# Kernel tuning notes

Measured on AMD Instinct MI355X. Metric: run time of the kernel, lower is better.

## Reference

```python
import jax, jax.numpy as jnp
import numpy as np
from math import comb

G, NPG, D = 32, 128, 128   # graphs, nodes-per-graph, hidden dim
N = G * NPG                # 4096 nodes per side
E = 65536                  # edges per side (avg degree 16)
K = 6                      # Bernstein order (bern_k)
S, DCONV, DTR = 16, 4, 8   # mamba d_state, d_conv, dt_rank
HE = 27
SIGMAS = [1.0, 10.0, 100.0, 1000.0, 10000.0]


def _leaky(x, s=0.02):
    return jnp.where(x >= 0, x, s * x)


def _bnorm(x, g, b, eps=1e-5):
    m = jnp.mean(x, axis=0)
    v = jnp.var(x, axis=0)
    return (x - m) * jax.lax.rsqrt(v + eps) * g + b


def _bern_prop(x, src, dst, w, temp):
    # BernNet Bern_prop: Bernstein polynomial of sym-normalized Laplacian with weights relu(temp)
    n = x.shape[0]
    temp = jax.nn.relu(temp)
    deg = jax.ops.segment_sum(w, src, num_segments=n)
    dinv = jnp.where(deg > 0, 1.0 / jnp.sqrt(deg + 1e-12), 0.0)
    nw = (w * dinv[src] * dinv[dst])[:, None]
    adj = lambda v: jax.ops.segment_sum(nw * v[src], dst, num_segments=n)
    tmps = [x]
    xv = x
    for _ in range(K):
        xv = xv + adj(xv)          # (2I - L) v = v + A_norm v
        tmps.append(xv)
    out = (comb(K, 0) / 2 ** K) * temp[0] * tmps[K]
    for i in range(K):
        v = tmps[K - i - 1]
        for _ in range(i + 1):
            v = v - adj(v)         # L v = v - A_norm v
        out = out + (comb(K, i + 1) / 2 ** K) * temp[i + 1] * v
    return out


def _mamba(h, in_w, conv_w, conv_b, xproj_w, dt_w, dt_b, A_log, Dp, out_w):
    # Mamba block, d_model=D, expand=1 (d_inner=D), d_state=S, d_conv=DCONV
    Bb, L, _ = h.shape
    xq, z = jnp.split(h @ in_w, 2, axis=-1)             # [B,L,D] each
    xp = jnp.pad(xq, ((0, 0), (DCONV - 1, 0), (0, 0)))  # causal depthwise conv
    xc = conv_b + sum(xp[:, k:k + L, :] * conv_w[:, k] for k in range(DCONV))
    xc = jax.nn.silu(xc)
    dbl = xc @ xproj_w                                  # [B,L,DTR+2S]
    dt = jax.nn.softplus(dbl[..., :DTR] @ dt_w + dt_b)  # [B,L,D]
    Bm = dbl[..., DTR:DTR + S]
    Cm = dbl[..., DTR + S:]
    A = -jnp.exp(A_log)                                 # [D,S]
    dA = jnp.exp(dt[..., None] * A)                     # [B,L,D,S]
    dBx = dt[..., None] * Bm[:, :, None, :] * xc[..., None]

    def step(hs, ins):
        dA_t, dBx_t, C_t = ins
        hs = dA_t * hs + dBx_t
        return hs, jnp.einsum('bds,bs->bd', hs, C_t)

    h0 = jnp.zeros((Bb, D, S), h.dtype)
    _, ys = jax.lax.scan(step, h0, (jnp.swapaxes(dA, 0, 1),
                                    jnp.swapaxes(dBx, 0, 1),
                                    jnp.swapaxes(Cm, 0, 1)))
    y = jnp.swapaxes(ys, 0, 1) + xc * Dp
    return (y * jax.nn.silu(z)) @ out_w


def _xattn(q, k, v, mask):
    a = mask * (q @ k.T) - 1000.0 * (1.0 - mask)
    return jax.nn.softmax(a, axis=1) @ v


def setup_inputs():
    key = jax.random.key(0)
    ks = jax.random.split(key, 32)
    f = jnp.float32
    nrm = lambda k, shp, sc=1.0: jax.random.normal(k, shp, dtype=f) * sc
    h_lig = nrm(ks[0], (N, D), 0.5)
    h_rec = nrm(ks[1], (N, D), 0.5)
    x_lig = nrm(ks[2], (N, 3))
    x_rec = nrm(ks[3], (N, 3))
    he_1 = jax.random.uniform(ks[4], (E, HE), dtype=f)
    he_2 = jax.random.uniform(ks[5], (E, HE), dtype=f)
    g = (jnp.arange(E) // (E // G)).astype(jnp.int32)
    src1 = g * NPG + jax.random.randint(ks[6], (E,), 0, NPG, dtype=jnp.int32)
    dst1 = g * NPG + jax.random.randint(ks[7], (E,), 0, NPG, dtype=jnp.int32)
    src2 = g * NPG + jax.random.randint(ks[8], (E,), 0, NPG, dtype=jnp.int32)
    dst2 = g * NPG + jax.random.randint(ks[9], (E,), 0, NPG, dtype=jnp.int32)
    edge_index_1 = jnp.stack([src1, dst1])
    edge_index_2 = jnp.stack([src2, dst2])
    batch = (jnp.arange(N) // NPG).astype(jnp.int32)
    rng = np.random.default_rng(0)
    def mkperm(src):
        # lexsort([deg + noise, batch]) with batch as primary key
        deg = np.bincount(np.asarray(src), minlength=N).astype(np.float32)
        return jnp.asarray(np.lexsort((deg + rng.random(N).astype(np.float32),
                                       np.asarray(batch))).astype(np.int32))
    perm_1 = mkperm(src1)
    perm_2 = mkperm(src2)
    p = {}
    p['emlp_w1'] = nrm(ks[10], (32, D), 0.1)
    p['emlp_b1'] = jnp.zeros((D,), f)
    p['emlp_bn_g'] = jnp.ones((D,), f)
    p['emlp_bn_b'] = jnp.zeros((D,), f)
    p['emlp_w2'] = nrm(ks[11], (D, 1), 0.1)
    p['emlp_b2'] = jnp.zeros((1,), f)
    p['bern_temp'] = jnp.ones((K + 1,), f)
    p['m_in_w'] = nrm(ks[12], (D, 2 * D), 0.05)
    p['m_conv_w'] = nrm(ks[13], (D, DCONV), 0.2)
    p['m_conv_b'] = jnp.zeros((D,), f)
    p['m_xproj_w'] = nrm(ks[14], (D, DTR + 2 * S), 0.05)
    p['m_dt_w'] = nrm(ks[15], (DTR, D), 0.2)
    p['m_dt_b'] = jnp.full((D,), -4.0, f)
    p['m_A_log'] = jnp.log(jnp.broadcast_to(jnp.arange(1, S + 1, dtype=f), (D, S)))
    p['m_D'] = jnp.ones((D,), f)
    p['m_out_w'] = nrm(ks[16], (D, D), 0.05)
    p['q_w'] = nrm(ks[17], (D, D), 0.05)
    p['k_w'] = nrm(ks[18], (D, D), 0.05)
    p['v_w'] = nrm(ks[19], (D, D), 0.05)
    p['bn1_g'] = jnp.ones((D,), f)
    p['bn1_b'] = jnp.zeros((D,), f)
    p['bn2_g'] = jnp.ones((D,), f)
    p['bn2_b'] = jnp.zeros((D,), f)
    p['ff_w1'] = nrm(ks[20], (D, 2 * D), 0.05)
    p['ff_b1'] = jnp.zeros((2 * D,), f)
    p['ff_w2'] = nrm(ks[21], (2 * D, D), 0.05)
    p['ff_b2'] = jnp.zeros((D,), f)
    return dict(h_lig=h_lig, h_rec=h_rec, x_lig=x_lig, x_rec=x_rec,
                he_1=he_1, he_2=he_2, **p,
                edge_index_1=edge_index_1, edge_index_2=edge_index_2,
                batch_1=batch, batch_2=batch, perm_1=perm_1, perm_2=perm_2)


def reference(h_lig, h_rec, x_lig, x_rec, he_1, he_2,
              emlp_w1, emlp_b1, emlp_bn_g, emlp_bn_b, emlp_w2, emlp_b2,
              bern_temp, m_in_w, m_conv_w, m_conv_b, m_xproj_w, m_dt_w,
              m_dt_b, m_A_log, m_D, m_out_w, q_w, k_w, v_w,
              bn1_g, bn1_b, bn2_g, bn2_b, ff_w1, ff_b1, ff_w2, ff_b2,
              edge_index_1, edge_index_2, batch_1, batch_2, perm_1, perm_2):

    def side(h, x, he, ei, perm):
        src, dst = ei[0], ei[1]
        d2 = jnp.sum((x[src] - x[dst]) ** 2, axis=1, keepdims=True)
        ew = jnp.concatenate([jnp.exp(-d2 / s) for s in SIGMAS], axis=1)  # [E,5]
        t = _leaky(jnp.concatenate([ew, he], axis=1) @ emlp_w1 + emlp_b1)
        t = _bnorm(t, emlp_bn_g, emlp_bn_b)
        w = jax.nn.relu(t @ emlp_w2 + emlp_b2)[:, 0]                      # [E]
        h_local = _bern_prop(h, src, dst, w, bern_temp)
        inv = jnp.argsort(perm)
        hd = h[perm].reshape(G, NPG, D)   # uniform graph sizes -> exact dense batch
        ha = _mamba(hd, m_in_w, m_conv_w, m_conv_b, m_xproj_w, m_dt_w,
                    m_dt_b, m_A_log, m_D, m_out_w).reshape(N, D)[inv]
        return _bnorm(h + h_local + ha, bn1_g, bn1_b)

    hl = side(h_lig, x_lig, he_1, edge_index_1, perm_1)
    hr = side(h_rec, x_rec, he_2, edge_index_2, perm_2)
    mask = (batch_1[:, None] == batch_2[None, :]).astype(hl.dtype)
    cl = _xattn(_leaky(hl @ q_w), _leaky(hr @ k_w), hr @ v_w, mask)
    cr = _xattn(_leaky(hr @ q_w), _leaky(hl @ k_w), hl @ v_w, mask.T)
    hl = hl + cl
    hr = hr + cr
    ff = lambda h: jax.nn.relu(h @ ff_w1 + ff_b1) @ ff_w2 + ff_b2
    hl = _bnorm(hl + ff(hl), bn2_g, bn2_b)
    hr = _bnorm(hr + ff(hr), bn2_g, bn2_b)
    return hl, hr
```

## Files before the change

kernel.cpp:

```cpp
#include <hip/hip_runtime.h>
#include <math.h>

#define G_    32
#define NPG_  128
#define D_    128
#define N_    4096
#define E_    65536
#define ND_   (N_*D_)

#define W_OFF     0
#define DEG_OFF   65536
#define STATS_OFF 69632
#define BUF0      71680
#define HL_OFF    (BUF0 + 0*ND_)
#define HA_OFF    (BUF0 + 1*ND_)
#define X1_OFF    (BUF0 + 2*ND_)
#define HMID_OFF  (BUF0 + 3*ND_)
#define XC_OFF    (BUF0 + 4*ND_)
#define DTB_OFF   (BUF0 + 5*ND_)
#define YB_OFF    (BUF0 + 6*ND_)
#define XZ_OFF    (BUF0 + 7*ND_)
#define DBL_OFF   (BUF0 + 9*ND_)
#define WT_OFF    (DBL_OFF + N_*40)
#define SS_       ((size_t)(WT_OFF + 4096))

__device__ __forceinline__ float leakyf(float x){ return x >= 0.f ? x : 0.02f*x; }
__device__ __forceinline__ float siluf (float x){ return x / (1.f + expf(-x)); }

__device__ __forceinline__ void edge_feat(const float* __restrict__ x,
                                          const float* __restrict__ he,
                                          const int* __restrict__ ei,
                                          int e, float* feat, int& sN, int& dN)
{
  sN = ei[e]; dN = ei[E_ + e];
  float dx = x[sN*3+0]-x[dN*3+0];
  float dy = x[sN*3+1]-x[dN*3+1];
  float dz = x[sN*3+2]-x[dN*3+2];
  float d2 = dx*dx + dy*dy + dz*dz;
  feat[0] = expf(-d2);
  feat[1] = expf(d2 * -0.1f);
  feat[2] = expf(d2 * -0.01f);
  feat[3] = expf(d2 * -0.001f);
  feat[4] = expf(d2 * -0.0001f);
#pragma unroll
  for (int j = 0; j < 27; ++j) feat[5+j] = he[(size_t)e*27 + j];
}

__global__ void wt_kernel(const float* __restrict__ w1, float* __restrict__ wt)
{
  for (int k = threadIdx.x; k < 4096; k += 256) {
    int c = k >> 5, j = k & 31;
    wt[k] = w1[j*128 + c];
  }
}

__global__ __launch_bounds__(256, 2)
void edge_stats_kernel(const float* __restrict__ xl, const float* __restrict__ xr,
                       const float* __restrict__ hel, const float* __restrict__ her,
                       const int* __restrict__ ei1, const int* __restrict__ ei2,
                       const float* __restrict__ wt, const float* __restrict__ b1,
                       float* __restrict__ ws)
{
  int side = blockIdx.y;
  const float* x  = side ? xr  : xl;
  const float* he = side ? her : hel;
  const int*   ei = side ? ei2 : ei1;
  float* stats = ws + (size_t)side*SS_ + STATS_OFF;
  __shared__ float featL[256][36];
  __shared__ float lstat[256];
  int tid = threadIdx.x;

  {
    int sN, dN; float feat[32];
    edge_feat(x, he, ei, blockIdx.x*256 + tid, feat, sN, dN);
#pragma unroll
    for (int j4 = 0; j4 < 8; ++j4)
      *(float4*)&featL[tid][j4*4] = *(float4*)&feat[j4*4];
  }
  lstat[tid] = 0.f;
  __syncthreads();

  int w    = tid >> 6;
  int lane = tid & 63;
  int es   = lane >> 5;
  int cg   = lane & 31;
  float4 wr[4][8];
  float  b1r[4];
#pragma unroll
  for (int c = 0; c < 4; ++c) {
    b1r[c] = b1[4*cg + c];
#pragma unroll
    for (int j4 = 0; j4 < 8; ++j4)
      wr[c][j4] = *(const float4*)&wt[(4*cg + c)*32 + j4*4];
  }
  float s1[4] = {0.f,0.f,0.f,0.f}, s2[4] = {0.f,0.f,0.f,0.f};
  int ebase = w*64 + es*32;
  for (int i = 0; i < 32; ++i) {
    const float* fr = featL[ebase + i];
    float4 f[8];
#pragma unroll
    for (int j4 = 0; j4 < 8; ++j4) f[j4] = *(const float4*)&fr[j4*4];
#pragma unroll
    for (int c = 0; c < 4; ++c) {
      float acc = b1r[c];
#pragma unroll
      for (int j4 = 0; j4 < 8; ++j4) {
        float4 w4 = wr[c][j4];
        acc += f[j4].x*w4.x + f[j4].y*w4.y + f[j4].z*w4.z + f[j4].w*w4.w;
      }
      float t = leakyf(acc);
      s1[c] += t; s2[c] += t*t;
    }
  }
#pragma unroll
  for (int c = 0; c < 4; ++c) {
    s1[c] += __shfl_xor(s1[c], 32, 64);
    s2[c] += __shfl_xor(s2[c], 32, 64);
  }
  if (es == 0) {
#pragma unroll
    for (int c = 0; c < 4; ++c) {
      atomicAdd(&lstat[4*cg + c],       s1[c]);
      atomicAdd(&lstat[128 + 4*cg + c], s2[c]);
    }
  }
  __syncthreads();
  atomicAdd(&stats[tid], lstat[tid]);
}

__global__ void edge_finalize_kernel(const float* __restrict__ g_, const float* __restrict__ b_,
                                     const float* __restrict__ w2, const float* __restrict__ b2,
                                     float* __restrict__ ws)
{
  int side = blockIdx.y;
  float* stats = ws + (size_t)side*SS_ + STATS_OFF;
  __shared__ float red[128];
  int c = threadIdx.x;
  const float invE = 1.f/(float)E_;
  float mean = stats[c]*invE;
  float var  = fmaxf(stats[128+c]*invE - mean*mean, 0.f);
  float scale = rsqrtf(var + 1e-5f) * g_[c];
  stats[256+c] = scale * w2[c];
  red[c] = (b_[c] - mean*scale) * w2[c];
  __syncthreads();
  for (int off = 64; off; off >>= 1) { if (c < off) red[c] += red[c+off]; __syncthreads(); }
  if (c == 0) stats[384] = red[0] + b2[0];
}

__global__ __launch_bounds__(256, 2)
void edge_w_kernel(const float* __restrict__ xl, const float* __restrict__ xr,
                   const float* __restrict__ hel, const float* __restrict__ her,
                   const int* __restrict__ ei1, const int* __restrict__ ei2,
                   const float* __restrict__ wt, const float* __restrict__ b1,
                   float* __restrict__ ws)
{
  int side = blockIdx.y;
  const float* x  = side ? xr  : xl;
  const float* he = side ? her : hel;
  const int*   ei = side ? ei2 : ei1;
  float* base = ws + (size_t)side*SS_;
  const float* stats = base + STATS_OFF;
  float* wbuf = base + W_OFF;
  float* deg  = base + DEG_OFF;
  __shared__ float featL[256][36];
  int tid = threadIdx.x;

  {
    int sN, dN; float feat[32];
    edge_feat(x, he, ei, blockIdx.x*256 + tid, feat, sN, dN);
#pragma unroll
    for (int j4 = 0; j4 < 8; ++j4)
      *(float4*)&featL[tid][j4*4] = *(float4*)&feat[j4*4];
    *(int*)&featL[tid][32] = sN;
  }
  __syncthreads();

  int w    = tid >> 6;
  int lane = tid & 63;
  int es   = lane >> 5;
  int cg   = lane & 31;
  float4 wr[4][8];
  float  b1r[4], al[4];
#pragma unroll
  for (int c = 0; c < 4; ++c) {
    b1r[c] = b1[4*cg + c];
    al[c]  = stats[256 + 4*cg + c];
#pragma unroll
    for (int j4 = 0; j4 < 8; ++j4)
      wr[c][j4] = *(const float4*)&wt[(4*cg + c)*32 + j4*4];
  }
  float beta = stats[384];
  int ebase = w*64 + es*32;
  for (int i = 0; i < 32; ++i) {
    const float* fr = featL[ebase + i];
    float4 f[8];
#pragma unroll
    for (int j4 = 0; j4 < 8; ++j4) f[j4] = *(const float4*)&fr[j4*4];
    float p = 0.f;
#pragma unroll
    for (int c = 0; c < 4; ++c) {
      float acc = b1r[c];
#pragma unroll
      for (int j4 = 0; j4 < 8; ++j4) {
        float4 w4 = wr[c][j4];
        acc += f[j4].x*w4.x + f[j4].y*w4.y + f[j4].z*w4.z + f[j4].w*w4.w;
      }
      p += leakyf(acc) * al[c];
    }
    p += __shfl_xor(p, 1, 32);
    p += __shfl_xor(p, 2, 32);
    p += __shfl_xor(p, 4, 32);
    p += __shfl_xor(p, 8, 32);
    p += __shfl_xor(p, 16, 32);
    if (cg == 0) {
      int e = blockIdx.x*256 + ebase + i;
      float wv = fmaxf(beta + p, 0.f);
      wbuf[e] = wv;
      int sN = *(const int*)&featL[ebase + i][32];
      atomicAdd(&deg[sN], wv);
    }
  }
}

__global__ __launch_bounds__(256)
void bern_horner_kernel(const float* __restrict__ hl_in, const float* __restrict__ hr_in,
                        const int* __restrict__ ei1, const int* __restrict__ ei2,
                        const float* __restrict__ bern_temp, float* __restrict__ ws)
{
  int side = blockIdx.y;
  int g  = blockIdx.x >> 2;
  int d0 = (blockIdx.x & 3) * 32;
  const float* h  = side ? hr_in : hl_in;
  const int*   ei = side ? ei2 : ei1;
  float* base = ws + (size_t)side*SS_;
  const float* wbuf = base + W_OFF;
  const float* deg  = base + DEG_OFF;
  float* hloc = base + HL_OFF;

  __shared__ float A[128*132];
  __shared__ float v[128*32];
  int tid = threadIdx.x;
  for (int i = tid; i < 128*132; i += 256) A[i] = 0.f;

  const float btab[7][7] = {
    { 1,  6, 15,  20, 15,  6,  1},
    { 1,  4,  5,   0, -5, -4, -1},
    { 1,  2, -1,  -4, -1,  2,  1},
    { 1,  0, -3,   0,  3,  0, -1},
    { 1, -2, -1,   4, -1, -2,  1},
    { 1, -4,  5,   0, -5,  4, -1},
    { 1, -6, 15, -20, 15, -6,  1}};
  const float comb6[7] = {1,6,15,20,15,6,1};
  float a[7];
#pragma unroll
  for (int m = 0; m < 7; ++m) a[m] = 0.f;
#pragma unroll
  for (int j = 0; j < 7; ++j) {
    float tj = fmaxf(bern_temp[j], 0.f) * comb6[j] * (1.f/64.f);
#pragma unroll
    for (int m = 0; m < 7; ++m) a[m] += tj * btab[j][m];
  }
  __syncthreads();

  int ebase = g*2048, nbase = g*128;
  for (int i = tid; i < 2048; i += 256) {
    int e = ebase + i;
    int sN = ei[e], dN = ei[E_ + e];
    float ds_ = deg[sN], dd_ = deg[dN];
    float aa = ds_ > 0.f ? rsqrtf(ds_ + 1e-12f) : 0.f;
    float bb = dd_ > 0.f ? rsqrtf(dd_ + 1e-12f) : 0.f;
    atomicAdd(&A[(dN - nbase)*132 + (sN - nbase)], wbuf[e]*aa*bb);
  }

  const int db = (tid & 7)*4;
  const int rb = (tid >> 3)*4;
  float hreg[4][4], r[4][4], t[4][4];
#pragma unroll
  for (int i = 0; i < 4; ++i) {
    float4 h4 = *(const float4*)&h[(size_t)(nbase + rb + i)*128 + d0 + db];
    hreg[i][0]=h4.x; hreg[i][1]=h4.y; hreg[i][2]=h4.z; hreg[i][3]=h4.w;
#pragma unroll
    for (int jj = 0; jj < 4; ++jj) r[i][jj] = a[6]*hreg[i][jj];
  }

  for (int step = 5; step >= 0; --step) {
    __syncthreads();
#pragma unroll
    for (int i = 0; i < 4; ++i)
      *(float4*)&v[(rb+i)*32 + db] = make_float4(r[i][0], r[i][1], r[i][2], r[i][3]);
    __syncthreads();
#pragma unroll
    for (int i = 0; i < 4; ++i)
#pragma unroll
      for (int jj = 0; jj < 4; ++jj) t[i][jj] = 0.f;
    for (int k = 0; k < 128; k += 4) {
      float4 V0 = *(const float4*)&v[(k+0)*32 + db];
      float4 V1 = *(const float4*)&v[(k+1)*32 + db];
      float4 V2 = *(const float4*)&v[(k+2)*32 + db];
      float4 V3 = *(const float4*)&v[(k+3)*32 + db];
#pragma unroll
      for (int i = 0; i < 4; ++i) {
        float4 A4 = *(const float4*)&A[(rb+i)*132 + k];
        t[i][0] += A4.x*V0.x + A4.y*V1.x + A4.z*V2.x + A4.w*V3.x;
        t[i][1] += A4.x*V0.y + A4.y*V1.y + A4.z*V2.y + A4.w*V3.y;
        t[i][2] += A4.x*V0.z + A4.y*V1.z + A4.z*V2.z + A4.w*V3.z;
        t[i][3] += A4.x*V0.w + A4.y*V1.w + A4.z*V2.w + A4.w*V3.w;
      }
    }
    float ak = a[step];
#pragma unroll
    for (int i = 0; i < 4; ++i)
#pragma unroll
      for (int jj = 0; jj < 4; ++jj) r[i][jj] = t[i][jj] + ak*hreg[i][jj];
  }

#pragma unroll
  for (int i = 0; i < 4; ++i)
    *(float4*)&hloc[(size_t)(nbase + rb + i)*128 + d0 + db] =
        make_float4(r[i][0], r[i][1], r[i][2], r[i][3]);
}

template<int K, int NC, int TC, int CSPLIT, int ACT, int GATHER, int SCATTER, int ADDC, int BIAS>
__global__ __launch_bounds__(256)
void gemm_kernel(const float* __restrict__ A0, const float* __restrict__ A1, int lda,
                 const float* __restrict__ W, const float* __restrict__ bias,
                 float* __restrict__ C0, float* __restrict__ C1, int ldc,
                 const int* __restrict__ idx0, const int* __restrict__ idx1,
                 const float* __restrict__ add0, const float* __restrict__ add1)
{
  int side = blockIdx.y;
  const float* A = side ? A1 : A0;
  float* C = side ? C1 : C0;
  const int* idx = side ? idx1 : idx0;
  const float* addsrc = side ? add1 : add0;
  constexpr int RPT = TC/8;
  constexpr int CLEN = NC/CSPLIT;
  __shared__ float Alds[32][K];
  __shared__ float Wlds[K][TC];
  const int tid = threadIdx.x;
  const int r0 = (blockIdx.x / CSPLIT) * 32;
  const int cbase = (blockIdx.x % CSPLIT) * CLEN;
  for (int i = tid*4; i < 32*K; i += 1024) {
    int r = i / K, k = i % K;
    int row = GATHER ? idx[r0 + r] : (r0 + r);
    *(float4*)&Alds[r][k] = *(const float4*)&A[(size_t)row*lda + k];
  }
  for (int c0 = cbase; c0 < cbase + CLEN; c0 += TC) {
    __syncthreads();
    for (int i = tid*4; i < K*TC; i += 1024) {
      int k = i / TC, c = i % TC;
      if (c0 + c < NC) *(float4*)&Wlds[k][c] = *(const float4*)&W[k*NC + c0 + c];
      else             *(float4*)&Wlds[k][c] = make_float4(0.f,0.f,0.f,0.f);
    }
    __syncthreads();
    const int cl = tid % TC;
    const int rsub = (tid / TC) * RPT;
    float accv[RPT];
#pragma unroll
    for (int j = 0; j < RPT; ++j) accv[j] = 0.f;
    for (int k = 0; k < K; k += 4) {
      float w0 = Wlds[k][cl], w1v = Wlds[k+1][cl], w2v = Wlds[k+2][cl], w3v = Wlds[k+3][cl];
#pragma unroll
      for (int j = 0; j < RPT; ++j) {
        float4 a4 = *(const float4*)&Alds[rsub+j][k];
        accv[j] += a4.x*w0 + a4.y*w1v + a4.z*w2v + a4.w*w3v;
      }
    }
    int c = c0 + cl;
    if (c < NC) {
#pragma unroll
      for (int j = 0; j < RPT; ++j) {
        int row  = r0 + rsub + j;
        int orow = SCATTER ? idx[row] : row;
        float vv = accv[j];
        if (BIAS)     vv += bias[c];
        if (ACT == 1) vv = leakyf(vv);
        if (ACT == 2) vv = fmaxf(vv, 0.f);
        if (ADDC)     vv += addsrc[(size_t)orow*ldc + c];
        C[(size_t)orow*ldc + c] = vv;
      }
    }
  }
}

__global__ __launch_bounds__(256)
void qkv_kernel(const float* __restrict__ qw, const float* __restrict__ kw,
                const float* __restrict__ vw, float* __restrict__ ws)
{
  int side = blockIdx.y;
  int mat  = blockIdx.z;
  float* base = ws + (size_t)side*SS_;
  const float* A = base + HMID_OFF;
  const float* W = mat == 0 ? qw : (mat == 1 ? kw : vw);
  float* C = base + (mat == 0 ? XC_OFF : (mat == 1 ? DTB_OFF : YB_OFF));
  __shared__ float Alds[32][128];
  __shared__ float Wlds[128][64];
  const int tid = threadIdx.x;
  const int r0 = (blockIdx.x >> 1) * 32;
  const int c0 = (blockIdx.x & 1) * 64;
  for (int i = tid*4; i < 32*128; i += 1024)
    *(float4*)&Alds[i>>7][i&127] = *(const float4*)&A[(size_t)(r0 + (i>>7))*128 + (i&127)];
  for (int i = tid*4; i < 128*64; i += 1024)
    *(float4*)&Wlds[i>>6][i&63] = *(const float4*)&W[(i>>6)*128 + c0 + (i&63)];
  __syncthreads();
  const int cl = tid & 63;
  const int rsub = (tid >> 6) * 8;
  float accv[8];
#pragma unroll
  for (int j = 0; j < 8; ++j) accv[j] = 0.f;
  for (int k = 0; k < 128; k += 4) {
    float w0 = Wlds[k][cl], w1v = Wlds[k+1][cl], w2v = Wlds[k+2][cl], w3v = Wlds[k+3][cl];
#pragma unroll
    for (int j = 0; j < 8; ++j) {
      float4 a4 = *(const float4*)&Alds[rsub+j][k];
      accv[j] += a4.x*w0 + a4.y*w1v + a4.z*w2v + a4.w*w3v;
    }
  }
#pragma unroll
  for (int j = 0; j < 8; ++j) {
    float vv = accv[j];
    if (mat < 2) vv = leakyf(vv);
    C[(size_t)(r0 + rsub + j)*128 + c0 + cl] = vv;
  }
}

__global__ __launch_bounds__(256)
void conv_kernel(const float* __restrict__ cw, const float* __restrict__ cb, float* __restrict__ ws)
{
  int side = blockIdx.y;
  float* base = ws + (size_t)side*SS_;
  const float* xz = base + XZ_OFF;
  float* xc = base + XC_OFF;
  int i = blockIdx.x*256 + threadIdx.x;
  int j = i >> 7, d = i & 127;
  int l = j & 127;
  float a = cb[d];
#pragma unroll
  for (int k = 0; k < 4; ++k) {
    int ll = l - 3 + k;
    if (ll >= 0) a += xz[(size_t)(j-3+k)*256 + d] * cw[d*4 + k];
  }
  xc[i] = siluf(a);
}

__global__ __launch_bounds__(256)
void scan_kernel(const float* __restrict__ A_log, const float* __restrict__ Dp,
                 const float* __restrict__ dtw, const float* __restrict__ dtbias,
                 float* __restrict__ ws)
{
  int side = blockIdx.z;
  int g  = blockIdx.x;
  int d0 = blockIdx.y * 16;
  float* base = ws + (size_t)side*SS_;
  const float* dbl = base + DBL_OFF;
  const float* xcb = base + XC_OFF;
  float* xz = base + XZ_OFF;

  __shared__ float ldbl[128][40];
  __shared__ float lxc[128][16];
  __shared__ float ldt[128][16];
  __shared__ float lz[128][16];
  __shared__ float ly[128][16];
  __shared__ float ltw[8][16];
  __shared__ float ltb[16];

  int tid = threadIdx.x;
  int rowbase = g*128;
  if (tid < 128)      ltw[tid>>4][tid&15] = dtw[(tid>>4)*128 + d0 + (tid&15)];
  else if (tid < 144) ltb[tid-128] = dtbias[d0 + (tid-128)];
  for (int i = tid; i < 128*40; i += 256)
    ((float*)ldbl)[i] = dbl[(size_t)rowbase*40 + i];
  for (int i = tid; i < 2048; i += 256) {
    int l = i >> 4, dd = i & 15;
    lxc[l][dd] = xcb[(size_t)(rowbase+l)*128 + d0 + dd];
    lz[l][dd]  = xz[(size_t)(rowbase+l)*256 + 128 + d0 + dd];
  }
  __syncthreads();
  for (int i = tid; i < 2048; i += 256) {
    int l = i >> 4, dd = i & 15;
    float a = ltb[dd];
#pragma unroll
    for (int k = 0; k < 8; ++k) a += ldbl[l][k]*ltw[k][dd];
    ldt[l][dd] = a > 20.f ? a : log1pf(expf(a));
  }
  __syncthreads();

  int s = tid & 15, dl = (tid >> 4) & 15;
  float Ac  = -expf(A_log[(d0+dl)*16 + s]);
  float dpv = Dp[d0+dl];
  float hsv = 0.f;
  for (int l = 0; l < 128; ++l) {
    float dtv = ldt[l][dl];
    float xcv = lxc[l][dl];
    float Bv  = ldbl[l][8+s];
    float Cv  = ldbl[l][24+s];
    hsv = expf(dtv*Ac)*hsv + (dtv*xcv)*Bv;
    float val = hsv*Cv;
    val += __shfl_xor(val, 1, 16);
    val += __shfl_xor(val, 2, 16);
    val += __shfl_xor(val, 4, 16);
    val += __shfl_xor(val, 8, 16);
    if (s == 0) ly[l][dl] = val + xcv*dpv;
  }
  __syncthreads();
  for (int i = tid; i < 2048; i += 256) {
    int l = i >> 4, dd = i & 15;
    float y = ly[l][dd];
    float z = lz[l][dd];
    xz[(size_t)(rowbase+l)*256 + d0 + dd] = y * siluf(z);
  }
}

__global__ __launch_bounds__(256)
void stats_kernel(const float* __restrict__ hl_in, const float* __restrict__ hr_in,
                  float* __restrict__ ws, int mode, int statsoff)
{
  int side = blockIdx.y;
  float* base = ws + (size_t)side*SS_;
  const float* h    = side ? hr_in : hl_in;
  const float* hloc = base + HL_OFF;
  const float* ha   = base + HA_OFF;
  float* x1 = base + X1_OFF;
  float* stats = base + STATS_OFF + statsoff;
  int tid = threadIdx.x;
  int c = tid & 127;
  float s1 = 0.f, s2 = 0.f;
  for (int it = 0; it < 16; ++it) {
    int r = blockIdx.x*32 + (tid >> 7) + it*2;
    size_t i = (size_t)r*128 + c;
    float v;
    if (mode == 0) { v = h[i] + hloc[i] + ha[i]; x1[i] = v; }
    else           { v = ha[i]; }
    s1 += v; s2 += v*v;
  }
  __shared__ float red[256];
  red[tid] = s1; __syncthreads();
  if (tid < 128) atomicAdd(&stats[tid], red[tid] + red[tid+128]);
  __syncthreads();
  red[tid] = s2; __syncthreads();
  if (tid < 128) atomicAdd(&stats[128+tid], red[tid] + red[tid+128]);
}

__global__ void bn_finalize_kernel(const float* __restrict__ g_, const float* __restrict__ b_,
                                   float* __restrict__ ws, int statsoff, float invM)
{
  int side = blockIdx.y;
  float* stats = ws + (size_t)side*SS_ + STATS_OFF + statsoff;
  int c = threadIdx.x;
  float mean = stats[c]*invM;
  float var  = fmaxf(stats[128+c]*invM - mean*mean, 0.f);
  float scale = rsqrtf(var + 1e-5f) * g_[c];
  stats[256+c] = scale;
  stats[384+c] = b_[c] - mean*scale;
}

__global__ __launch_bounds__(256)
void bn_apply_kernel(float* __restrict__ ws, float* __restrict__ dout,
                     int srcoff, int dstoff, int statsoff, int to_dout)
{
  int side = blockIdx.y;
  float* base = ws + (size_t)side*SS_;
  const float* src = base + srcoff;
  const float* stats = base + STATS_OFF + statsoff;
  float* dst = to_dout ? (dout + (size_t)side*ND_) : (base + dstoff);
  size_t i = (size_t)blockIdx.x*256 + threadIdx.x;
  int c = (int)(i & 127);
  dst[i] = src[i]*stats[256+c] + stats[384+c];
}

__global__ __launch_bounds__(256)
void attn_kernel(float* __restrict__ ws)
{
  int dir = blockIdx.z;
  int g   = blockIdx.x;
  int rt  = blockIdx.y;
  float* baseq = ws + (size_t)dir*SS_;
  float* basek = ws + (size_t)(1-dir)*SS_;
  const float* qb = baseq + XC_OFF;
  const float* kb = basek + DTB_OFF;
  const float* vb = basek + YB_OFF;
  const float* hm = baseq + HMID_OFF;
  float* h2 = baseq + X1_OFF;

  __shared__ float KT[128][132];
  __shared__ float Qs[32][132];
  __shared__ float sp[32][132];

  const int tid = threadIdx.x;
  const int cl  = tid & 31;
  const int r0  = (tid >> 5) * 4;
  const int c0  = cl * 4;
  const int rowg = g*128 + rt*32;

  {
    const float* qsrc = qb + (size_t)rowg*128;
    for (int i = tid; i < 32*32; i += 256) {
      int r = i >> 5, d4 = i & 31;
      *(float4*)&Qs[r][d4*4] = *(const float4*)&qsrc[(size_t)r*128 + d4*4];
    }
  }
  {
    const float* ksrc = kb + (size_t)(g*128)*128;
    for (int i = tid; i < 128*32; i += 256) {
      int d4 = i >> 7, n = i & 127;
      float4 k4 = *(const float4*)&ksrc[(size_t)n*128 + d4*4];
      KT[d4*4+0][n] = k4.x;
      KT[d4*4+1][n] = k4.y;
      KT[d4*4+2][n] = k4.z;
      KT[d4*4+3][n] = k4.w;
    }
  }
  __syncthreads();

  float acc[4][4];
#pragma unroll
  for (int i = 0; i < 4; ++i)
#pragma unroll
    for (int j = 0; j < 4; ++j) acc[i][j] = 0.f;

  for (int d = 0; d < 128; d += 4) {
    float4 k0 = *(const float4*)&KT[d+0][c0];
    float4 k1 = *(const float4*)&KT[d+1][c0];
    float4 k2 = *(const float4*)&KT[d+2][c0];
    float4 k3 = *(const float4*)&KT[d+3][c0];
#pragma unroll
    for (int i = 0; i < 4; ++i) {
      float4 q4 = *(const float4*)&Qs[r0+i][d];
      acc[i][0] += q4.x*k0.x + q4.y*k1.x + q4.z*k2.x + q4.w*k3.x;
      acc[i][1] += q4.x*k0.y + q4.y*k1.y + q4.z*k2.y + q4.w*k3.y;
      acc[i][2] += q4.x*k0.z + q4.y*k1.z + q4.z*k2.z + q4.w*k3.z;
      acc[i][3] += q4.x*k0.w + q4.y*k1.w + q4.z*k2.w + q4.w*k3.w;
    }
  }

  float inv[4];
#pragma unroll
  for (int i = 0; i < 4; ++i) {
    float m = fmaxf(fmaxf(acc[i][0], acc[i][1]), fmaxf(acc[i][2], acc[i][3]));
#pragma unroll
    for (int off = 1; off < 32; off <<= 1) m = fmaxf(m, __shfl_xor(m, off, 32));
    float p0 = expf(acc[i][0]-m), p1 = expf(acc[i][1]-m);
    float p2 = expf(acc[i][2]-m), p3 = expf(acc[i][3]-m);
    float s = p0 + p1 + p2 + p3;
#pragma unroll
    for (int off = 1; off < 32; off <<= 1) s += __shfl_xor(s, off, 32);
    inv[i] = 1.f/s;
    *(float4*)&sp[r0+i][c0] = make_float4(p0, p1, p2, p3);
  }
  __syncthreads();

  {
    const float* vsrc = vb + (size_t)(g*128)*128;
    for (int i = tid; i < 128*32; i += 256) {
      int n = i >> 5, d4 = i & 31;
      *(float4*)&KT[n][d4*4] = *(const float4*)&vsrc[(size_t)n*128 + d4*4];
    }
  }
  __syncthreads();

  float o[4][4];
#pragma unroll
  for (int i = 0; i < 4; ++i)
#pragma unroll
    for (int j = 0; j < 4; ++j) o[i][j] = 0.f;

  for (int n = 0; n < 128; n += 4) {
    float4 v0 = *(const float4*)&KT[n+0][c0];
    float4 v1 = *(const float4*)&KT[n+1][c0];
    float4 v2 = *(const float4*)&KT[n+2][c0];
    float4 v3 = *(const float4*)&KT[n+3][c0];
#pragma unroll
    for (int i = 0; i < 4; ++i) {
      float4 p4 = *(const float4*)&sp[r0+i][n];
      o[i][0] += p4.x*v0.x + p4.y*v1.x + p4.z*v2.x + p4.w*v3.x;
      o[i][1] += p4.x*v0.y + p4.y*v1.y + p4.z*v2.y + p4.w*v3.y;
      o[i][2] += p4.x*v0.z + p4.y*v1.z + p4.z*v2.z + p4.w*v3.z;
      o[i][3] += p4.x*v0.w + p4.y*v1.w + p4.z*v2.w + p4.w*v3.w;
    }
  }

#pragma unroll
  for (int i = 0; i < 4; ++i) {
    size_t off = (size_t)(rowg + r0 + i)*128 + c0;
    float4 hm4 = *(const float4*)&hm[off];
    float4 r4;
    r4.x = hm4.x + o[i][0]*inv[i];
    r4.y = hm4.y + o[i][1]*inv[i];
    r4.z = hm4.z + o[i][2]*inv[i];
    r4.w = hm4.w + o[i][3]*inv[i];
    *(float4*)&h2[off] = r4;
  }
}

extern "C" void kernel_launch(void* const* d_in, const int* in_sizes, int n_in,
                              void* d_out, int out_size, void* d_ws, size_t ws_size,
                              hipStream_t stream)
{
  const float* h_lig     = (const float*)d_in[0];
  const float* h_rec     = (const float*)d_in[1];
  const float* x_lig     = (const float*)d_in[2];
  const float* x_rec     = (const float*)d_in[3];
  const float* he_1      = (const float*)d_in[4];
  const float* he_2      = (const float*)d_in[5];
  const float* emlp_w1   = (const float*)d_in[6];
  const float* emlp_b1   = (const float*)d_in[7];
  const float* emlp_bn_g = (const float*)d_in[8];
  const float* emlp_bn_b = (const float*)d_in[9];
  const float* emlp_w2   = (const float*)d_in[10];
  const float* emlp_b2   = (const float*)d_in[11];
  const float* bern_temp = (const float*)d_in[12];
  const float* m_in_w    = (const float*)d_in[13];
  const float* m_conv_w  = (const float*)d_in[14];
  const float* m_conv_b  = (const float*)d_in[15];
  const float* m_xproj_w = (const float*)d_in[16];
  const float* m_dt_w    = (const float*)d_in[17];
  const float* m_dt_b    = (const float*)d_in[18];
  const float* m_A_log   = (const float*)d_in[19];
  const float* m_D       = (const float*)d_in[20];
  const float* m_out_w   = (const float*)d_in[21];
  const float* q_w       = (const float*)d_in[22];
  const float* k_w       = (const float*)d_in[23];
  const float* v_w       = (const float*)d_in[24];
  const float* bn1_g     = (const float*)d_in[25];
  const float* bn1_b     = (const float*)d_in[26];
  const float* bn2_g     = (const float*)d_in[27];
  const float* bn2_b     = (const float*)d_in[28];
  const float* ff_w1     = (const float*)d_in[29];
  const float* ff_b1     = (const float*)d_in[30];
  const float* ff_w2     = (const float*)d_in[31];
  const float* ff_b2     = (const float*)d_in[32];
  const int*   ei1       = (const int*)d_in[33];
  const int*   ei2       = (const int*)d_in[34];
  const int*   perm1     = (const int*)d_in[37];
  const int*   perm2     = (const int*)d_in[38];

  float* ws   = (float*)d_ws;
  float* dout = (float*)d_out;

#define B0(off) (ws + (size_t)(off))
#define B1(off) (ws + SS_ + (size_t)(off))

  for (int s = 0; s < 2; ++s)
    hipMemsetAsync((char*)d_ws + ((size_t)s*SS_ + DEG_OFF)*sizeof(float), 0,
                   (N_ + 2048)*sizeof(float), stream);

  wt_kernel<<<1, 256, 0, stream>>>(emlp_w1, B0(WT_OFF));
  edge_stats_kernel<<<dim3(256,2), 256, 0, stream>>>(x_lig,x_rec,he_1,he_2,ei1,ei2,B0(WT_OFF),emlp_b1,ws);
  edge_finalize_kernel<<<dim3(1,2), 128, 0, stream>>>(emlp_bn_g,emlp_bn_b,emlp_w2,emlp_b2,ws);
  edge_w_kernel<<<dim3(256,2), 256, 0, stream>>>(x_lig,x_rec,he_1,he_2,ei1,ei2,B0(WT_OFF),emlp_b1,ws);

  bern_horner_kernel<<<dim3(G_*4,2), 256, 0, stream>>>(h_lig,h_rec,ei1,ei2,bern_temp,ws);

  gemm_kernel<128,256,64,4,0,1,0,0,0><<<dim3(512,2),256,0,stream>>>(
      h_lig,h_rec,128, m_in_w,nullptr, B0(XZ_OFF),B1(XZ_OFF),256, perm1,perm2, nullptr,nullptr);
  conv_kernel<<<dim3(2048,2), 256, 0, stream>>>(m_conv_w,m_conv_b,ws);
  gemm_kernel<128,40,64,1,0,0,0,0,0><<<dim3(128,2),256,0,stream>>>(
      B0(XC_OFF),B1(XC_OFF),128, m_xproj_w,nullptr, B0(DBL_OFF),B1(DBL_OFF),40, nullptr,nullptr, nullptr,nullptr);
  scan_kernel<<<dim3(32,8,2), 256, 0, stream>>>(m_A_log,m_D,m_dt_w,m_dt_b,ws);
  gemm_kernel<128,128,64,2,0,0,1,0,0><<<dim3(256,2),256,0,stream>>>(
      B0(XZ_OFF),B1(XZ_OFF),256, m_out_w,nullptr, B0(HA_OFF),B1(HA_OFF),128, perm1,perm2, nullptr,nullptr);

  stats_kernel<<<dim3(128,2), 256, 0, stream>>>(h_lig,h_rec,ws,0,512);
  bn_finalize_kernel<<<dim3(1,2), 128, 0, stream>>>(bn1_g,bn1_b,ws,512,1.f/(float)N_);
  bn_apply_kernel<<<dim3(2048,2), 256, 0, stream>>>(ws,dout,X1_OFF,HMID_OFF,512,0);

  qkv_kernel<<<dim3(256,2,3), 256, 0, stream>>>(q_w,k_w,v_w,ws);
  attn_kernel<<<dim3(32,4,2), 256, 0, stream>>>(ws);

  gemm_kernel<128,256,64,4,2,0,0,0,1><<<dim3(512,2),256,0,stream>>>(
      B0(X1_OFF),B1(X1_OFF),128, ff_w1,ff_b1, B0(XZ_OFF),B1(XZ_OFF),256, nullptr,nullptr, nullptr,nullptr);
  gemm_kernel<256,128,32,4,0,0,0,1,1><<<dim3(512,2),256,0,stream>>>(
      B0(XZ_OFF),B1(XZ_OFF),256, ff_w2,ff_b2, B0(HA_OFF),B1(HA_OFF),128, nullptr,nullptr, B0(X1_OFF),B1(X1_OFF));
  stats_kernel<<<dim3(128,2), 256, 0, stream>>>(h_lig,h_rec,ws,1,1024);
  bn_finalize_kernel<<<dim3(1,2), 128, 0, stream>>>(bn2_g,bn2_b,ws,1024,1.f/(float)N_);
  bn_apply_kernel<<<dim3(2048,2), 256, 0, stream>>>(ws,dout,HA_OFF,0,1024,1);
}
```

Baseline: 457.7 us.

## Register-tile edge MLP over 4x4 blocks and cache edge features between passes

The edge MLP first layer in both edge kernels is restructured so that each thread computes a 4-edge by 4-channel tile, with the weight matrix staged in shared memory instead of per-thread registers. The transpose kernel goes away. The stats pass now writes the 32-float edge features to a workspace buffer (aliased onto the h_local region), and the weight pass reloads them instead of recomputing exps and gathers. This trades extra global traffic and shared memory for fewer recomputations and better register and data reuse, and it relies on the h_local buffer not being written until bern_horner runs.

```diff
diff --git a/kernel.cpp b/kernel.cpp
--- a/kernel.cpp
+++ b/kernel.cpp
@@ -23,6 +23,7 @@
 #define DBL_OFF   (BUF0 + 9*ND_)
 #define WT_OFF    (DBL_OFF + N_*40)
 #define SS_       ((size_t)(WT_OFF + 4096))
+#define FEAT_OFF  HL_OFF
 
 __device__ __forceinline__ float leakyf(float x){ return x >= 0.f ? x : 0.02f*x; }
 __device__ __forceinline__ float siluf (float x){ return x / (1.f + expf(-x)); }
@@ -46,86 +47,79 @@
   for (int j = 0; j < 27; ++j) feat[5+j] = he[(size_t)e*27 + j];
 }
 
-__global__ void wt_kernel(const float* __restrict__ w1, float* __restrict__ wt)
-{
-  for (int k = threadIdx.x; k < 4096; k += 256) {
-    int c = k >> 5, j = k & 31;
-    wt[k] = w1[j*128 + c];
-  }
-}
-
 __global__ __launch_bounds__(256, 2)
 void edge_stats_kernel(const float* __restrict__ xl, const float* __restrict__ xr,
                        const float* __restrict__ hel, const float* __restrict__ her,
                        const int* __restrict__ ei1, const int* __restrict__ ei2,
-                       const float* __restrict__ wt, const float* __restrict__ b1,
+                       const float* __restrict__ w1, const float* __restrict__ b1,
                        float* __restrict__ ws)
 {
   int side = blockIdx.y;
   const float* x  = side ? xr  : xl;
   const float* he = side ? her : hel;
   const int*   ei = side ? ei2 : ei1;
-  float* stats = ws + (size_t)side*SS_ + STATS_OFF;
+  float* base  = ws + (size_t)side*SS_;
+  float* stats = base + STATS_OFF;
+  float* featbuf = base + FEAT_OFF;
   __shared__ float featL[256][36];
-  __shared__ float lstat[256];
+  __shared__ float Wl[32][128];
+  __shared__ float bstat[256];
   int tid = threadIdx.x;
+
+  for (int i = tid*4; i < 4096; i += 1024)
+    *(float4*)&Wl[i>>7][i&127] = *(const float4*)&w1[i];
+  bstat[tid] = 0.f;
 
   {
     int sN, dN; float feat[32];
     edge_feat(x, he, ei, blockIdx.x*256 + tid, feat, sN, dN);
-#pragma unroll
-    for (int j4 = 0; j4 < 8; ++j4)
+    float* fb = &featbuf[(size_t)(blockIdx.x*256 + tid)*32];
+#pragma unroll
+    for (int j4 = 0; j4 < 8; ++j4) {
       *(float4*)&featL[tid][j4*4] = *(float4*)&feat[j4*4];
-  }
-  lstat[tid] = 0.f;
-  __syncthreads();
-
-  int w    = tid >> 6;
-  int lane = tid & 63;
-  int es   = lane >> 5;
-  int cg   = lane & 31;
-  float4 wr[4][8];
-  float  b1r[4];
+      *(float4*)&fb[j4*4]         = *(float4*)&feat[j4*4];
+    }
+  }
+  __syncthreads();
+
+  int eg0 = tid >> 5, cg = tid & 31;
+  float4 b1v = *(const float4*)&b1[4*cg];
+  float s1[4] = {0.f,0.f,0.f,0.f}, s2[4] = {0.f,0.f,0.f,0.f};
+  for (int j = 0; j < 8; ++j) {
+    int e0 = (eg0 + 8*j)*4;
+    float z[4][4];
+#pragma unroll
+    for (int e = 0; e < 4; ++e) { z[e][0]=b1v.x; z[e][1]=b1v.y; z[e][2]=b1v.z; z[e][3]=b1v.w; }
+#pragma unroll
+    for (int k = 0; k < 32; k += 4) {
+      float4 w0 = *(const float4*)&Wl[k+0][4*cg];
+      float4 w1q= *(const float4*)&Wl[k+1][4*cg];
+      float4 w2q= *(const float4*)&Wl[k+2][4*cg];
+      float4 w3q= *(const float4*)&Wl[k+3][4*cg];
+#pragma unroll
+      for (int e = 0; e < 4; ++e) {
+        float4 a = *(const float4*)&featL[e0+e][k];
+        z[e][0] += a.x*w0.x + a.y*w1q.x + a.z*w2q.x + a.w*w3q.x;
+        z[e][1] += a.x*w0.y + a.y*w1q.y + a.z*w2q.y + a.w*w3q.y;
+        z[e][2] += a.x*w0.z + a.y*w1q.z + a.z*w2q.z + a.w*w3q.z;
+        z[e][3] += a.x*w0.w + a.y*w1q.w + a.z*w2q.w + a.w*w3q.w;
+      }
+    }
+#pragma unroll
+    for (int e = 0; e < 4; ++e)
+#pragma unroll
+      for (int c = 0; c < 4; ++c) {
+        float t = leakyf(z[e][c]);
+        s1[c] += t; s2[c] += t*t;
+      }
+  }
 #pragma unroll
   for (int c = 0; c < 4; ++c) {
-    b1r[c] = b1[4*cg + c];
-#pragma unroll
-    for (int j4 = 0; j4 < 8; ++j4)
-      wr[c][j4] = *(const float4*)&wt[(4*cg + c)*32 + j4*4];
-  }
-  float s1[4] = {0.f,0.f,0.f,0.f}, s2[4] = {0.f,0.f,0.f,0.f};
-  int ebase = w*64 + es*32;
-  for (int i = 0; i < 32; ++i) {
-    const float* fr = featL[ebase + i];
-    float4 f[8];
-#pragma unroll
-    for (int j4 = 0; j4 < 8; ++j4) f[j4] = *(const float4*)&fr[j4*4];
-#pragma unroll
-    for (int c = 0; c < 4; ++c) {
-      float acc = b1r[c];
-#pragma unroll
-      for (int j4 = 0; j4 < 8; ++j4) {
-        float4 w4 = wr[c][j4];
-        acc += f[j4].x*w4.x + f[j4].y*w4.y + f[j4].z*w4.z + f[j4].w*w4.w;
-      }
-      float t = leakyf(acc);
-      s1[c] += t; s2[c] += t*t;
-    }
-  }
-#pragma unroll
-  for (int c = 0; c < 4; ++c) {
-    s1[c] += __shfl_xor(s1[c], 32, 64);
-    s2[c] += __shfl_xor(s2[c], 32, 64);
-  }
-  if (es == 0) {
-#pragma unroll
-    for (int c = 0; c < 4; ++c) {
-      atomicAdd(&lstat[4*cg + c],       s1[c]);
-      atomicAdd(&lstat[128 + 4*cg + c], s2[c]);
-    }
-  }
-  __syncthreads();
-  atomicAdd(&stats[tid], lstat[tid]);
+    atomicAdd(&bstat[4*cg + c],       s1[c]);
+    atomicAdd(&bstat[128 + 4*cg + c], s2[c]);
+  }
+  __syncthreads();
+  atomicAdd(&stats[tid], bstat[tid]);
 }
 
 __global__ void edge_finalize_kernel(const float* __restrict__ g_, const float* __restrict__ b_,
@@ -148,76 +142,77 @@
 }
 
 __global__ __launch_bounds__(256, 2)
-void edge_w_kernel(const float* __restrict__ xl, const float* __restrict__ xr,
-                   const float* __restrict__ hel, const float* __restrict__ her,
-                   const int* __restrict__ ei1, const int* __restrict__ ei2,
-                   const float* __restrict__ wt, const float* __restrict__ b1,
+void edge_w_kernel(const int* __restrict__ ei1, const int* __restrict__ ei2,
+                   const float* __restrict__ w1, const float* __restrict__ b1,
                    float* __restrict__ ws)
 {
   int side = blockIdx.y;
-  const float* x  = side ? xr  : xl;
-  const float* he = side ? her : hel;
-  const int*   ei = side ? ei2 : ei1;
+  const int* ei = side ? ei2 : ei1;
   float* base = ws + (size_t)side*SS_;
   const float* stats = base + STATS_OFF;
+  const float* featbuf = base + FEAT_OFF;
   float* wbuf = base + W_OFF;
   float* deg  = base + DEG_OFF;
   __shared__ float featL[256][36];
+  __shared__ float Wl[32][128];
   int tid = threadIdx.x;
 
+  for (int i = tid*4; i < 4096; i += 1024)
+    *(float4*)&Wl[i>>7][i&127] = *(const float4*)&w1[i];
   {
-    int sN, dN; float feat[32];
-    edge_feat(x, he, ei, blockIdx.x*256 + tid, feat, sN, dN);
-#pragma unroll
-    for (int j4 = 0; j4 < 8; ++j4)
-      *(float4*)&featL[tid][j4*4] = *(float4*)&feat[j4*4];
-    *(int*)&featL[tid][32] = sN;
-  }
-  __syncthreads();
-
-  int w    = tid >> 6;
-  int lane = tid & 63;
-  int es   = lane >> 5;
-  int cg   = lane & 31;
-  float4 wr[4][8];
-  float  b1r[4], al[4];
-#pragma unroll
-  for (int c = 0; c < 4; ++c) {
-    b1r[c] = b1[4*cg + c];
-    al[c]  = stats[256 + 4*cg + c];
-#pragma unroll
-    for (int j4 = 0; j4 < 8; ++j4)
-      wr[c][j4] = *(const float4*)&wt[(4*cg + c)*32 + j4*4];
-  }
+    const float* fb = featbuf + (size_t)blockIdx.x*256*32;
+    for (int i = tid; i < 2048; i += 256) {
+      float4 f4 = *(const float4*)&fb[i*4];
+      *(float4*)&featL[i>>3][(i&7)*4] = f4;
+    }
+  }
+  __syncthreads();
+
+  int eg0 = tid >> 5, cg = tid & 31;
+  float4 b1v = *(const float4*)&b1[4*cg];
+  float4 al4 = *(const float4*)&stats[256 + 4*cg];
   float beta = stats[384];
-  int ebase = w*64 + es*32;
-  for (int i = 0; i < 32; ++i) {
-    const float* fr = featL[ebase + i];
-    float4 f[8];
-#pragma unroll
-    for (int j4 = 0; j4 < 8; ++j4) f[j4] = *(const float4*)&fr[j4*4];
-    float p = 0.f;
-#pragma unroll
-    for (int c = 0; c < 4; ++c) {
-      float acc = b1r[c];
-#pragma unroll
-      for (int j4 = 0; j4 < 8; ++j4) {
-        float4 w4 = wr[c][j4];
-        acc += f[j4].x*w4.x + f[j4].y*w4.y + f[j4].z*w4.z + f[j4].w*w4.w;
+  for (int j = 0; j < 8; ++j) {
+    int e0 = (eg0 + 8*j)*4;
+    float z[4][4];
+#pragma unroll
+    for (int e = 0; e < 4; ++e) { z[e][0]=b1v.x; z[e][1]=b1v.y; z[e][2]=b1v.z; z[e][3]=b1v.w; }
+#pragma unroll
+    for (int k = 0; k < 32; k += 4) {
+      float4 w0 = *(const float4*)&Wl[k+0][4*cg];
+      float4 w1q= *(const float4*)&Wl[k+1][4*cg];
+      float4 w2q= *(const float4*)&Wl[k+2][4*cg];
+      float4 w3q= *(const float4*)&Wl[k+3][4*cg];
+#pragma unroll
+      for (int e = 0; e < 4; ++e) {
+        float4 a = *(const float4*)&featL[e0+e][k];
+        z[e][0] += a.x*w0.x + a.y*w1q.x + a.z*w2q.x + a.w*w3q.x;
+        z[e][1] += a.x*w0.y + a.y*w1q.y + a.z*w2q.y + a.w*w3q.y;
+        z[e][2] += a.x*w0.z + a.y*w1q.z + a.z*w2q.z + a.w*w3q.z;
+        z[e][3] += a.x*w0.w + a.y*w1q.w + a.z*w2q.w + a.w*w3q.w;
       }
-      p += leakyf(acc) * al[c];
-    }
-    p += __shfl_xor(p, 1, 32);
-    p += __shfl_xor(p, 2, 32);
-    p += __shfl_xor(p, 4, 32);
-    p += __shfl_xor(p, 8, 32);
-    p += __shfl_xor(p, 16, 32);
+    }
+    float p[4];
+#pragma unroll
+    for (int e = 0; e < 4; ++e)
+      p[e] = leakyf(z[e][0])*al4.x + leakyf(z[e][1])*al4.y
+           + leakyf(z[e][2])*al4.z + leakyf(z[e][3])*al4.w;
+#pragma unroll
+    for (int e = 0; e < 4; ++e) {
+      p[e] += __shfl_xor(p[e], 1, 32);
+      p[e] += __shfl_xor(p[e], 2, 32);
+      p[e] += __shfl_xor(p[e], 4, 32);
+      p[e] += __shfl_xor(p[e], 8, 32);
+      p[e] += __shfl_xor(p[e], 16, 32);
+    }
     if (cg == 0) {
-      int e = blockIdx.x*256 + ebase + i;
-      float wv = fmaxf(beta + p, 0.f);
-      wbuf[e] = wv;
-      int sN = *(const int*)&featL[ebase + i][32];
-      atomicAdd(&deg[sN], wv);
+#pragma unroll
+      for (int e = 0; e < 4; ++e) {
+        int eg = blockIdx.x*256 + e0 + e;
+        float wv = fmaxf(beta + p[e], 0.f);
+        wbuf[eg] = wv;
+        atomicAdd(&deg[ei[eg]], wv);
+      }
     }
   }
 }
@@ -744,10 +739,9 @@
     hipMemsetAsync((char*)d_ws + ((size_t)s*SS_ + DEG_OFF)*sizeof(float), 0,
                    (N_ + 2048)*sizeof(float), stream);
 
-  wt_kernel<<<1, 256, 0, stream>>>(emlp_w1, B0(WT_OFF));
-  edge_stats_kernel<<<dim3(256,2), 256, 0, stream>>>(x_lig,x_rec,he_1,he_2,ei1,ei2,B0(WT_OFF),emlp_b1,ws);
+  edge_stats_kernel<<<dim3(256,2), 256, 0, stream>>>(x_lig,x_rec,he_1,he_2,ei1,ei2,emlp_w1,emlp_b1,ws);
   edge_finalize_kernel<<<dim3(1,2), 128, 0, stream>>>(emlp_bn_g,emlp_bn_b,emlp_w2,emlp_b2,ws);
-  edge_w_kernel<<<dim3(256,2), 256, 0, stream>>>(x_lig,x_rec,he_1,he_2,ei1,ei2,B0(WT_OFF),emlp_b1,ws);
+  edge_w_kernel<<<dim3(256,2), 256, 0, stream>>>(ei1,ei2,emlp_w1,emlp_b1,ws);
 
   bern_horner_kernel<<<dim3(G_*4,2), 256, 0, stream>>>(h_lig,h_rec,ei1,ei2,bern_temp,ws);
 
```

After: 501.9 us. +9.7%, slower.
